# Kernel optimization log

Hardware: AMD Instinct MI355X
Metric: run time of the kernel (lower is better)

The kernel has to match this reference:

```python
import jax, jax.numpy as jnp
import numpy as np

B, S, E, H = 8, 1024, 64, 8
DK = E // H  # n_wires per head
DIM = 2 ** DK  # statevector size


def _quantum_projection(x, phi):
    """Faithful batched simulation of _QLayer for every (batch, seq, head).
    Encoder RX(x_i) followed by trainable RX(phi_i) on the same wire equals
    RX(x_i + phi_i). Then a CNOT ring, then <Z_w> for each wire.
    x: [B,S,E] float, phi: [H,DK] float -> [B,S,E] float expectations.
    """
    b, s, e = x.shape
    theta = x.reshape(b, s, H, DK) + phi  # [B,S,H,DK]
    M = b * s * H
    th = theta.reshape(M, DK)
    # RX(t)|0> = cos(t/2)|0> - i sin(t/2)|1>
    c = jnp.cos(th * 0.5).astype(jnp.complex64)
    sn = (jnp.sin(th * 0.5) * (-1j)).astype(jnp.complex64)
    q = jnp.stack([c, sn], axis=-1)  # [M, DK, 2]
    # product state via iterated kron over the DK wires (fixed small loop)
    amps = jnp.ones((M, 1), jnp.complex64)
    for w in range(DK):
        amps = (amps[:, :, None] * q[:, w, None, :]).reshape(M, -1)
    st = amps.reshape((M,) + (2,) * DK)
    # CNOT ring: (0,1),(1,2),...,(DK-2,DK-1),(DK-1,0)
    gates = [(w, w + 1) for w in range(DK - 1)] + [(DK - 1, 0)]
    for cw, tw in gates:
        ac = 1 + cw
        s0 = jnp.take(st, 0, axis=ac)  # control = 0: identity
        s1 = jnp.take(st, 1, axis=ac)  # control = 1: flip target
        at = 1 + tw - (1 if tw > cw else 0)  # target axis after removing control axis
        s1 = jnp.flip(s1, axis=at)
        st = jnp.stack([s0, s1], axis=ac)
    stf = st.reshape(M, DIM)
    probs = stf.real ** 2 + stf.imag ** 2  # [M, DIM]
    # <Z_w> = sum_k probs[k] * (1 - 2*bit_w(k)); wire 0 is most-significant bit
    bits = (jnp.arange(DIM)[:, None] >> jnp.arange(DK - 1, -1, -1)[None, :]) & 1
    signs = (1 - 2 * bits).astype(probs.dtype)  # [DIM, DK]
    expz = probs @ signs  # [M, DK]
    return expz.reshape(b, s, e)


def setup_inputs() -> dict:
    key = jax.random.key(0)
    k1, k2, k3, k4 = jax.random.split(key, 4)
    x = jax.random.normal(k1, (B, S, E), dtype=jnp.float32)
    phi = jax.random.normal(k2, (H, DK), dtype=jnp.float32) * 0.1  # trainable RX params
    lim = 1.0 / np.sqrt(E)
    W = jax.random.uniform(k3, (E, E), jnp.float32, -lim, lim)  # combine Linear weight
    b = jax.random.uniform(k4, (E,), jnp.float32, -lim, lim)    # combine Linear bias
    return {"x": x, "phi": phi, "W": W, "b": b}


def reference(x, phi, W, b):
    # q = k = v = _projection(x): the original calls _projection(x) 3 times with
    # the same params and no randomness, so they are identical; compute once.
    proj = _quantum_projection(x, phi)  # [B,S,E]
    scores = jax.nn.softmax(
        jnp.einsum('bse,bte->bst', proj, proj) / jnp.sqrt(jnp.float32(DK)), axis=-1)
    # dropout is identity in eval mode
    ctx = jnp.einsum('bst,bte->bse', scores, proj)
    return ctx @ W.T + b
```

## Files before the change

### kernel.cpp

```cpp
#include <hip/hip_runtime.h>
#include <hip/hip_bf16.h>

#define BB 8
#define SS 1024
#define EE 64
#define HH 8
#define DKW 8

typedef __hip_bfloat16 bf16;
typedef unsigned short u16;
typedef _Float16 half8v __attribute__((ext_vector_type(8)));
typedef float floatx4 __attribute__((ext_vector_type(4)));

#define MFMA16(a, b, c) __builtin_amdgcn_mfma_f32_16x16x32_f16(a, b, c, 0, 0, 0)

#define OFF_PROJT ((size_t)BB * SS * EE * 2)

template <int NT>
__device__ __forceinline__ bool detect_f32(const u16* __restrict__ base,
                                           int tid, int* red) {
    int cnt = 0;
#pragma unroll
    for (int i = tid; i < 2048; i += NT) {
        u16 u = base[i * 2];
        int ex = (u >> 7) & 0xFF;
        cnt += (ex >= 0x84) ? 1 : 0;
    }
#pragma unroll
    for (int off = 32; off > 0; off >>= 1) cnt += __shfl_xor(cnt, off, 64);
    if ((tid & 63) == 0) red[tid >> 6] = cnt;
    __syncthreads();
    int tot = 0;
#pragma unroll
    for (int w = 0; w < NT / 64; ++w) tot += red[w];
    return tot > 64;
}

__device__ __forceinline__ void proj_compute(const void* x, const void* phi,
                                             bool f32, int m, float* z) {
    int h = m & (HH - 1);
    float th[DKW];
    if (f32) {
        const float4* xp = (const float4*)((const float*)x + (size_t)m * DKW);
        const float4* pp = (const float4*)((const float*)phi + h * DKW);
        float4 x0 = xp[0], x1 = xp[1];
        float4 p0 = pp[0], p1 = pp[1];
        th[0] = x0.x + p0.x; th[1] = x0.y + p0.y; th[2] = x0.z + p0.z; th[3] = x0.w + p0.w;
        th[4] = x1.x + p1.x; th[5] = x1.y + p1.y; th[6] = x1.z + p1.z; th[7] = x1.w + p1.w;
    } else {
        union { uint4 u; bf16 hv[8]; } xu, pu;
        xu.u = *(const uint4*)((const bf16*)x + (size_t)m * DKW);
        pu.u = *(const uint4*)((const bf16*)phi + (size_t)h * DKW);
#pragma unroll
        for (int j = 0; j < DKW; ++j)
            th[j] = __bfloat162float(xu.hv[j]) + __bfloat162float(pu.hv[j]);
    }
    float c[DKW];
#pragma unroll
    for (int j = 0; j < DKW; ++j) c[j] = __cosf(th[j]);
    float suf = c[1];
#pragma unroll
    for (int j = 2; j < DKW; ++j) suf *= c[j];
    z[0] = suf;
    float pre = c[0];
#pragma unroll
    for (int w = 1; w < DKW; ++w) { pre *= c[w]; z[w] = pre; }
}

__global__ __launch_bounds__(256) void proj_f16_kernel(const void* __restrict__ x,
                                                       const void* __restrict__ phi,
                                                       _Float16* __restrict__ projH,
                                                       _Float16* __restrict__ projT) {
    __shared__ int redd[4];
    __shared__ _Float16 zt[EE][40];
    const int tid = threadIdx.x;
    const bool f32 = detect_f32<256>((const u16*)x, tid, redd);

    const int m = blockIdx.x * 256 + tid;
    float z[DKW];
    proj_compute(x, phi, f32, m, z);

    union { half8v v; _Float16 h[8]; } o;
#pragma unroll
    for (int j = 0; j < DKW; ++j) o.h[j] = (_Float16)z[j];
    *(half8v*)(projH + (size_t)m * DKW) = o.v;

    const int h = m & (HH - 1);
    const int sl = (tid >> 3) & 31;
#pragma unroll
    for (int j = 0; j < DKW; ++j) zt[h * DKW + j][sl] = o.h[j];
    __syncthreads();

    const int b = blockIdx.x >> 5;
    const int s0 = (blockIdx.x * 32) & (SS - 1);
    const int row = tid >> 2, ch = tid & 3;
    half8v vv = *(const half8v*)(&zt[row][ch * 8]);
    *(half8v*)(projT + ((size_t)(b * EE + row)) * SS + s0 + ch * 8) = vv;
}

__device__ __forceinline__ int sidx(int row, int colblk) {
    return row * 1024 + ((colblk ^ (row & 7)) << 3);
}

__global__ __launch_bounds__(512) void fused_attn(const _Float16* __restrict__ projH,
                                                  const _Float16* __restrict__ projT,
                                                  const void* __restrict__ Wp,
                                                  const void* __restrict__ biasp,
                                                  void* __restrict__ outp) {
    __shared__ _Float16 Stile[16 * 1024];
    __shared__ float    pacc[4][16][17];
    __shared__ _Float16 ctx_lds[16][72];
    __shared__ float    rowsum[16];
    __shared__ int      redd[8];

    const int tid = threadIdx.x;
    const int wave = tid >> 6, lane = tid & 63;
    const int lr = lane & 15, quad = lane >> 4;
    const int b = blockIdx.y;
    const int m0 = blockIdx.x * 16;

    const bool f32 = detect_f32<512>((const u16*)Wp, tid, redd);

    const _Float16* Pb = projH + (size_t)b * SS * EE;
    const float scale = 0.35355339059327373f;

    {
        const _Float16* arow = Pb + (size_t)(m0 + lr) * EE;
        half8v a0 = *(const half8v*)(arow + quad * 8);
        half8v a1 = *(const half8v*)(arow + 32 + quad * 8);
#pragma unroll 4
        for (int c = 0; c < 8; ++c) {
            int n = wave * 128 + c * 16;
            const _Float16* brow = Pb + (size_t)(n + lr) * EE;
            half8v b0 = *(const half8v*)(brow + quad * 8);
            half8v b1 = *(const half8v*)(brow + 32 + quad * 8);
            floatx4 acc = {0.f, 0.f, 0.f, 0.f};
            acc = MFMA16(a0, b0, acc);
            acc = MFMA16(a1, b1, acc);
#pragma unroll
            for (int r = 0; r < 4; ++r) {
                int row = quad * 4 + r, col = n + lr;
                Stile[sidx(row, col >> 3) + (col & 7)] = (_Float16)(acc[r] * scale);
            }
        }
    }
    __syncthreads();

    {
        const int row = tid >> 5, seg = tid & 31;
        half8v hv[4];
#pragma unroll
        for (int i = 0; i < 4; ++i)
            hv[i] = *(const half8v*)(&Stile[sidx(row, i * 32 + seg)]);
        float mloc = -1e30f;
#pragma unroll
        for (int i = 0; i < 4; ++i)
#pragma unroll
            for (int j = 0; j < 8; ++j) mloc = fmaxf(mloc, (float)hv[i][j]);
#pragma unroll
        for (int off = 16; off > 0; off >>= 1)
            mloc = fmaxf(mloc, __shfl_xor(mloc, off, 64));
        float lsum = 0.f;
#pragma unroll
        for (int i = 0; i < 4; ++i) {
#pragma unroll
            for (int j = 0; j < 8; ++j) {
                float e = __expf((float)hv[i][j] - mloc);
                lsum += e;
                hv[i][j] = (_Float16)(e * 256.f);
            }
        }
#pragma unroll
        for (int off = 16; off > 0; off >>= 1)
            lsum += __shfl_xor(lsum, off, 64);
        if (seg == 0) rowsum[row] = lsum;
#pragma unroll
        for (int i = 0; i < 4; ++i)
            *(half8v*)(&Stile[sidx(row, i * 32 + seg)]) = hv[i];
    }
    __syncthreads();

    const int khalf = wave >> 2, colg = wave & 3;
    floatx4 accT;
    {
        const _Float16* vrow = projT + ((size_t)(b * EE + colg * 16 + lr)) * SS
                               + khalf * 512;
        const int sbase = khalf * 64;
        floatx4 acc0 = {0.f, 0.f, 0.f, 0.f};
        floatx4 acc1 = {0.f, 0.f, 0.f, 0.f};
#pragma unroll 4
        for (int t = 0; t < 512; t += 64) {
            half8v aA = *(const half8v*)(&Stile[sidx(lr, sbase + (t >> 3) + quad)]);
            half8v vA = *(const half8v*)(vrow + t + quad * 8);
            half8v aB = *(const half8v*)(&Stile[sidx(lr, sbase + ((t + 32) >> 3) + quad)]);
            half8v vB = *(const half8v*)(vrow + t + 32 + quad * 8);
            acc0 = MFMA16(aA, vA, acc0);
            acc1 = MFMA16(aB, vB, acc1);
        }
        accT = acc0 + acc1;
    }
    if (khalf == 1) {
#pragma unroll
        for (int r = 0; r < 4; ++r) pacc[colg][quad * 4 + r][lr] = accT[r];
    }
    __syncthreads();
    if (khalf == 0) {
#pragma unroll
        for (int r = 0; r < 4; ++r) {
            int row_l = quad * 4 + r;
            float inv = 1.0f / (256.0f * rowsum[row_l]);
            ctx_lds[row_l][colg * 16 + lr] =
                (_Float16)((accT[r] + pacc[colg][row_l][lr]) * inv);
        }
    }
    __syncthreads();

    if (wave < 4) {
        const int o = wave * 16 + lr;
        half8v ca0 = *(const half8v*)(&ctx_lds[lr][quad * 8]);
        half8v ca1 = *(const half8v*)(&ctx_lds[lr][32 + quad * 8]);
        half8v wb0, wb1;
        if (f32) {
            const float* wr = (const float*)Wp + (size_t)o * EE;
            union { half8v v; _Float16 h[8]; } w0, w1;
#pragma unroll
            for (int j = 0; j < 8; ++j) {
                w0.h[j] = (_Float16)wr[quad * 8 + j];
                w1.h[j] = (_Float16)wr[32 + quad * 8 + j];
            }
            wb0 = w0.v; wb1 = w1.v;
        } else {
            const bf16* wr = (const bf16*)Wp + (size_t)o * EE;
            union { uint4 u; bf16 hv[8]; } r0, r1;
            r0.u = *(const uint4*)(wr + quad * 8);
            r1.u = *(const uint4*)(wr + 32 + quad * 8);
            union { half8v v; _Float16 h[8]; } w0, w1;
#pragma unroll
            for (int j = 0; j < 8; ++j) {
                w0.h[j] = (_Float16)__bfloat162float(r0.hv[j]);
                w1.h[j] = (_Float16)__bfloat162float(r1.hv[j]);
            }
            wb0 = w0.v; wb1 = w1.v;
        }
        floatx4 oacc = {0.f, 0.f, 0.f, 0.f};
        oacc = MFMA16(ca0, wb0, oacc);
        oacc = MFMA16(ca1, wb1, oacc);

        float bo = f32 ? ((const float*)biasp)[o]
                       : __bfloat162float(((const bf16*)biasp)[o]);
#pragma unroll
        for (int r = 0; r < 4; ++r) {
            size_t oi = ((size_t)b * SS + m0 + quad * 4 + r) * EE + o;
            float val = oacc[r] + bo;
            if (f32) ((float*)outp)[oi] = val;
            else     ((bf16*)outp)[oi] = __float2bfloat16(val);
        }
    }
}

extern "C" void kernel_launch(void* const* d_in, const int* in_sizes, int n_in,
                              void* d_out, int out_size, void* d_ws, size_t ws_size,
                              hipStream_t stream) {
    const void* x    = d_in[0];
    const void* phi  = d_in[1];
    const void* W    = d_in[2];
    const void* bias = d_in[3];

    _Float16* projH = (_Float16*)d_ws;
    _Float16* projT = (_Float16*)((char*)d_ws + OFF_PROJT);

    proj_f16_kernel<<<dim3(BB * SS * HH / 256), dim3(256), 0, stream>>>(x, phi, projH, projT);
    fused_attn<<<dim3(SS / 16, BB), dim3(512), 0, stream>>>(projH, projT, W, bias, d_out);
}
```

Baseline: 83.76 us.

## Fuse projection and attention into one cooperative kernel with grid sync

Merges the projection kernel and the fused attention kernel into a single cooperative launch of 512 blocks. Each block first computes its slice of projH/projT, then all blocks meet at a grid-wide barrier before running attention. The goal is to drop the second kernel launch and the gap between kernels. The cost is a grid-wide barrier, only 128 of 512 threads active during projection, and a cooperative launch that may fail; if it fails, the code falls back to the old two-kernel path.

```diff
diff --git a/kernel.cpp b/kernel.cpp
--- a/kernel.cpp
+++ b/kernel.cpp
@@ -1,5 +1,8 @@
 #include <hip/hip_runtime.h>
 #include <hip/hip_bf16.h>
+#include <hip/hip_cooperative_groups.h>
+
+namespace cg = cooperative_groups;
 
 #define BB 8
 #define SS 1024
@@ -20,7 +23,6 @@
 __device__ __forceinline__ bool detect_f32(const u16* __restrict__ base,
                                            int tid, int* red) {
     int cnt = 0;
-#pragma unroll
     for (int i = tid; i < 2048; i += NT) {
         u16 u = base[i * 2];
         int ex = (u >> 7) & 0xFF;
@@ -67,60 +69,57 @@
     for (int w = 1; w < DKW; ++w) { pre *= c[w]; z[w] = pre; }
 }
 
-__global__ __launch_bounds__(256) void proj_f16_kernel(const void* __restrict__ x,
-                                                       const void* __restrict__ phi,
-                                                       _Float16* __restrict__ projH,
-                                                       _Float16* __restrict__ projT) {
-    __shared__ int redd[4];
-    __shared__ _Float16 zt[EE][40];
-    const int tid = threadIdx.x;
-    const bool f32 = detect_f32<256>((const u16*)x, tid, redd);
-
-    const int m = blockIdx.x * 256 + tid;
-    float z[DKW];
-    proj_compute(x, phi, f32, m, z);
-
-    union { half8v v; _Float16 h[8]; } o;
-#pragma unroll
-    for (int j = 0; j < DKW; ++j) o.h[j] = (_Float16)z[j];
-    *(half8v*)(projH + (size_t)m * DKW) = o.v;
-
-    const int h = m & (HH - 1);
-    const int sl = (tid >> 3) & 31;
-#pragma unroll
-    for (int j = 0; j < DKW; ++j) zt[h * DKW + j][sl] = o.h[j];
-    __syncthreads();
-
-    const int b = blockIdx.x >> 5;
-    const int s0 = (blockIdx.x * 32) & (SS - 1);
-    const int row = tid >> 2, ch = tid & 3;
-    half8v vv = *(const half8v*)(&zt[row][ch * 8]);
-    *(half8v*)(projT + ((size_t)(b * EE + row)) * SS + s0 + ch * 8) = vv;
-}
-
 __device__ __forceinline__ int sidx(int row, int colblk) {
     return row * 1024 + ((colblk ^ (row & 7)) << 3);
 }
 
-__global__ __launch_bounds__(512) void fused_attn(const _Float16* __restrict__ projH,
-                                                  const _Float16* __restrict__ projT,
-                                                  const void* __restrict__ Wp,
-                                                  const void* __restrict__ biasp,
-                                                  void* __restrict__ outp) {
+__global__ __launch_bounds__(512, 4) void mega_kernel(const void* __restrict__ x,
+                                                      const void* __restrict__ phi,
+                                                      const void* __restrict__ Wp,
+                                                      const void* __restrict__ biasp,
+                                                      void* __restrict__ outp,
+                                                      _Float16* __restrict__ projH,
+                                                      _Float16* __restrict__ projT) {
     __shared__ _Float16 Stile[16 * 1024];
     __shared__ float    pacc[4][16][17];
     __shared__ _Float16 ctx_lds[16][72];
+    __shared__ _Float16 zt[EE][24];
     __shared__ float    rowsum[16];
     __shared__ int      redd[8];
 
     const int tid = threadIdx.x;
     const int wave = tid >> 6, lane = tid & 63;
     const int lr = lane & 15, quad = lane >> 4;
-    const int b = blockIdx.y;
-    const int m0 = blockIdx.x * 16;
-
-    const bool f32 = detect_f32<512>((const u16*)Wp, tid, redd);
-
+    const int blk = blockIdx.x;
+
+    const bool f32 = detect_f32<512>((const u16*)x, tid, redd);
+
+    {
+        if (tid < 128) {
+            int m = blk * 128 + tid;
+            float z[DKW];
+            proj_compute(x, phi, f32, m, z);
+            union { half8v v; _Float16 h[8]; } o;
+#pragma unroll
+            for (int j = 0; j < DKW; ++j) o.h[j] = (_Float16)z[j];
+            *(half8v*)(projH + (size_t)m * DKW) = o.v;
+            int h = m & (HH - 1), sl = tid >> 3;
+#pragma unroll
+            for (int j = 0; j < DKW; ++j) zt[h * DKW + j][sl] = o.h[j];
+        }
+        __syncthreads();
+        if (tid < 128) {
+            int pb = blk >> 6;
+            int s0 = (blk & 63) * 16;
+            int row = tid >> 1, ch = tid & 1;
+            half8v vv = *(const half8v*)(&zt[row][ch * 8]);
+            *(half8v*)(projT + ((size_t)(pb * EE + row)) * SS + s0 + ch * 8) = vv;
+        }
+    }
+    cg::this_grid().sync();
+
+    const int b = blk >> 6;
+    const int m0 = (blk & 63) * 16;
     const _Float16* Pb = projH + (size_t)b * SS * EE;
     const float scale = 0.35355339059327373f;
 
@@ -258,6 +257,191 @@
     }
 }
 
+__global__ __launch_bounds__(256) void proj_f16_kernel(const void* __restrict__ x,
+                                                       const void* __restrict__ phi,
+                                                       _Float16* __restrict__ projH,
+                                                       _Float16* __restrict__ projT) {
+    __shared__ int redd[4];
+    __shared__ _Float16 zt[EE][40];
+    const int tid = threadIdx.x;
+    const bool f32 = detect_f32<256>((const u16*)x, tid, redd);
+
+    const int m = blockIdx.x * 256 + tid;
+    float z[DKW];
+    proj_compute(x, phi, f32, m, z);
+
+    union { half8v v; _Float16 h[8]; } o;
+#pragma unroll
+    for (int j = 0; j < DKW; ++j) o.h[j] = (_Float16)z[j];
+    *(half8v*)(projH + (size_t)m * DKW) = o.v;
+
+    const int h = m & (HH - 1);
+    const int sl = (tid >> 3) & 31;
+#pragma unroll
+    for (int j = 0; j < DKW; ++j) zt[h * DKW + j][sl] = o.h[j];
+    __syncthreads();
+
+    const int b = blockIdx.x >> 5;
+    const int s0 = (blockIdx.x * 32) & (SS - 1);
+    const int row = tid >> 2, ch = tid & 3;
+    half8v vv = *(const half8v*)(&zt[row][ch * 8]);
+    *(half8v*)(projT + ((size_t)(b * EE + row)) * SS + s0 + ch * 8) = vv;
+}
+
+__global__ __launch_bounds__(512) void fused_attn(const _Float16* __restrict__ projH,
+                                                  const _Float16* __restrict__ projT,
+                                                  const void* __restrict__ Wp,
+                                                  const void* __restrict__ biasp,
+                                                  void* __restrict__ outp) {
+    __shared__ _Float16 Stile[16 * 1024];
+    __shared__ float    pacc[4][16][17];
+    __shared__ _Float16 ctx_lds[16][72];
+    __shared__ float    rowsum[16];
+    __shared__ int      redd[8];
+
+    const int tid = threadIdx.x;
+    const int wave = tid >> 6, lane = tid & 63;
+    const int lr = lane & 15, quad = lane >> 4;
+    const int b = blockIdx.y;
+    const int m0 = blockIdx.x * 16;
+
+    const bool f32 = detect_f32<512>((const u16*)Wp, tid, redd);
+    const _Float16* Pb = projH + (size_t)b * SS * EE;
+    const float scale = 0.35355339059327373f;
+
+    {
+        const _Float16* arow = Pb + (size_t)(m0 + lr) * EE;
+        half8v a0 = *(const half8v*)(arow + quad * 8);
+        half8v a1 = *(const half8v*)(arow + 32 + quad * 8);
+#pragma unroll 4
+        for (int c = 0; c < 8; ++c) {
+            int n = wave * 128 + c * 16;
+            const _Float16* brow = Pb + (size_t)(n + lr) * EE;
+            half8v b0 = *(const half8v*)(brow + quad * 8);
+            half8v b1 = *(const half8v*)(brow + 32 + quad * 8);
+            floatx4 acc = {0.f, 0.f, 0.f, 0.f};
+            acc = MFMA16(a0, b0, acc);
+            acc = MFMA16(a1, b1, acc);
+#pragma unroll
+            for (int r = 0; r < 4; ++r) {
+                int row = quad * 4 + r, col = n + lr;
+                Stile[sidx(row, col >> 3) + (col & 7)] = (_Float16)(acc[r] * scale);
+            }
+        }
+    }
+    __syncthreads();
+    {
+        const int row = tid >> 5, seg = tid & 31;
+        half8v hv[4];
+#pragma unroll
+        for (int i = 0; i < 4; ++i)
+            hv[i] = *(const half8v*)(&Stile[sidx(row, i * 32 + seg)]);
+        float mloc = -1e30f;
+#pragma unroll
+        for (int i = 0; i < 4; ++i)
+#pragma unroll
+            for (int j = 0; j < 8; ++j) mloc = fmaxf(mloc, (float)hv[i][j]);
+#pragma unroll
+        for (int off = 16; off > 0; off >>= 1)
+            mloc = fmaxf(mloc, __shfl_xor(mloc, off, 64));
+        float lsum = 0.f;
+#pragma unroll
+        for (int i = 0; i < 4; ++i) {
+#pragma unroll
+            for (int j = 0; j < 8; ++j) {
+                float e = __expf((float)hv[i][j] - mloc);
+                lsum += e;
+                hv[i][j] = (_Float16)(e * 256.f);
+            }
+        }
+#pragma unroll
+        for (int off = 16; off > 0; off >>= 1)
+            lsum += __shfl_xor(lsum, off, 64);
+        if (seg == 0) rowsum[row] = lsum;
+#pragma unroll
+        for (int i = 0; i < 4; ++i)
+            *(half8v*)(&Stile[sidx(row, i * 32 + seg)]) = hv[i];
+    }
+    __syncthreads();
+
+    const int khalf = wave >> 2, colg = wave & 3;
+    floatx4 accT;
+    {
+        const _Float16* vrow = projT + ((size_t)(b * EE + colg * 16 + lr)) * SS
+                               + khalf * 512;
+        const int sbase = khalf * 64;
+        floatx4 acc0 = {0.f, 0.f, 0.f, 0.f};
+        floatx4 acc1 = {0.f, 0.f, 0.f, 0.f};
+#pragma unroll 4
+        for (int t = 0; t < 512; t += 64) {
+            half8v aA = *(const half8v*)(&Stile[sidx(lr, sbase + (t >> 3) + quad)]);
+            half8v vA = *(const half8v*)(vrow + t + quad * 8);
+            half8v aB = *(const half8v*)(&Stile[sidx(lr, sbase + ((t + 32) >> 3) + quad)]);
+            half8v vB = *(const half8v*)(vrow + t + 32 + quad * 8);
+            acc0 = MFMA16(aA, vA, acc0);
+            acc1 = MFMA16(aB, vB, acc1);
+        }
+        accT = acc0 + acc1;
+    }
+    if (khalf == 1) {
+#pragma unroll
+        for (int r = 0; r < 4; ++r) pacc[colg][quad * 4 + r][lr] = accT[r];
+    }
+    __syncthreads();
+    if (khalf == 0) {
+#pragma unroll
+        for (int r = 0; r < 4; ++r) {
+            int row_l = quad * 4 + r;
+            float inv = 1.0f / (256.0f * rowsum[row_l]);
+            ctx_lds[row_l][colg * 16 + lr] =
+                (_Float16)((accT[r] + pacc[colg][row_l][lr]) * inv);
+        }
+    }
+    __syncthreads();
+
+    if (wave < 4) {
+        const int o = wave * 16 + lr;
+        half8v ca0 = *(const half8v*)(&ctx_lds[lr][quad * 8]);
+        half8v ca1 = *(const half8v*)(&ctx_lds[lr][32 + quad * 8]);
+        half8v wb0, wb1;
+        if (f32) {
+            const float* wr = (const float*)Wp + (size_t)o * EE;
+            union { half8v v; _Float16 h[8]; } w0, w1;
+#pragma unroll
+            for (int j = 0; j < 8; ++j) {
+                w0.h[j] = (_Float16)wr[quad * 8 + j];
+                w1.h[j] = (_Float16)wr[32 + quad * 8 + j];
+            }
+            wb0 = w0.v; wb1 = w1.v;
+        } else {
+            const bf16* wr = (const bf16*)Wp + (size_t)o * EE;
+            union { uint4 u; bf16 hv[8]; } r0, r1;
+            r0.u = *(const uint4*)(wr + quad * 8);
+            r1.u = *(const uint4*)(wr + 32 + quad * 8);
+            union { half8v v; _Float16 h[8]; } w0, w1;
+#pragma unroll
+            for (int j = 0; j < 8; ++j) {
+                w0.h[j] = (_Float16)__bfloat162float(r0.hv[j]);
+                w1.h[j] = (_Float16)__bfloat162float(r1.hv[j]);
+            }
+            wb0 = w0.v; wb1 = w1.v;
+        }
+        floatx4 oacc = {0.f, 0.f, 0.f, 0.f};
+        oacc = MFMA16(ca0, wb0, oacc);
+        oacc = MFMA16(ca1, wb1, oacc);
+
+        float bo = f32 ? ((const float*)biasp)[o]
+                       : __bfloat162float(((const bf16*)biasp)[o]);
+#pragma unroll
+        for (int r = 0; r < 4; ++r) {
+            size_t oi = ((size_t)b * SS + m0 + quad * 4 + r) * EE + o;
+            float val = oacc[r] + bo;
+            if (f32) ((float*)outp)[oi] = val;
+            else     ((bf16*)outp)[oi] = __float2bfloat16(val);
+        }
+    }
+}
+
 extern "C" void kernel_launch(void* const* d_in, const int* in_sizes, int n_in,
                               void* d_out, int out_size, void* d_ws, size_t ws_size,
                               hipStream_t stream) {
@@ -265,10 +449,20 @@
     const void* phi  = d_in[1];
     const void* W    = d_in[2];
     const void* bias = d_in[3];
+    void* outp = d_out;
 
     _Float16* projH = (_Float16*)d_ws;
     _Float16* projT = (_Float16*)((char*)d_ws + OFF_PROJT);
 
-    proj_f16_kernel<<<dim3(BB * SS * HH / 256), dim3(256), 0, stream>>>(x, phi, projH, projT);
-    fused_attn<<<dim3(SS / 16, BB), dim3(512), 0, stream>>>(projH, projT, W, bias, d_out);
-}
+    void* args[] = {(void*)&x, (void*)&phi, (void*)&W, (void*)&bias,
+                    (void*)&outp, (void*)&projH, (void*)&projT};
+    hipError_t err = hipLaunchCooperativeKernel(
+        reinterpret_cast<void*>(mega_kernel), dim3(512), dim3(512), args, 0, stream);
+
+    if (err != hipSuccess) {
+        proj_f16_kernel<<<dim3(BB * SS * HH / 256), dim3(256), 0, stream>>>(
+            x, phi, projH, projT);
+        fused_attn<<<dim3(SS / 16, BB), dim3(512), 0, stream>>>(
+            projH, projT, W, bias, d_out);
+    }
+}
```

Result: slower. 138.6 us (+65.5%).

## Fuse quantum projection into attention kernel, recomputing K/V tiles in shared memory

Applied to the files above, without the earlier changes.

Replaces the two-kernel pipeline with a single kernel that recomputes projected query, key and value tiles from x and phi directly into LDS, chunk by chunk, for both the QK and PV phases. This removes the workspace round trip and one kernel launch. In exchange, each block recomputes the projections of all keys twice, which multiplies the transcendental work and adds per-chunk barriers.

```diff
diff --git a/kernel.cpp b/kernel.cpp
--- a/kernel.cpp
+++ b/kernel.cpp
@@ -14,13 +14,10 @@
 
 #define MFMA16(a, b, c) __builtin_amdgcn_mfma_f32_16x16x32_f16(a, b, c, 0, 0, 0)
 
-#define OFF_PROJT ((size_t)BB * SS * EE * 2)
-
 template <int NT>
 __device__ __forceinline__ bool detect_f32(const u16* __restrict__ base,
                                            int tid, int* red) {
     int cnt = 0;
-#pragma unroll
     for (int i = tid; i < 2048; i += NT) {
         u16 u = base[i * 2];
         int ex = (u >> 7) & 0xFF;
@@ -67,46 +64,16 @@
     for (int w = 1; w < DKW; ++w) { pre *= c[w]; z[w] = pre; }
 }
 
-__global__ __launch_bounds__(256) void proj_f16_kernel(const void* __restrict__ x,
-                                                       const void* __restrict__ phi,
-                                                       _Float16* __restrict__ projH,
-                                                       _Float16* __restrict__ projT) {
-    __shared__ int redd[4];
-    __shared__ _Float16 zt[EE][40];
-    const int tid = threadIdx.x;
-    const bool f32 = detect_f32<256>((const u16*)x, tid, redd);
-
-    const int m = blockIdx.x * 256 + tid;
-    float z[DKW];
-    proj_compute(x, phi, f32, m, z);
-
-    union { half8v v; _Float16 h[8]; } o;
-#pragma unroll
-    for (int j = 0; j < DKW; ++j) o.h[j] = (_Float16)z[j];
-    *(half8v*)(projH + (size_t)m * DKW) = o.v;
-
-    const int h = m & (HH - 1);
-    const int sl = (tid >> 3) & 31;
-#pragma unroll
-    for (int j = 0; j < DKW; ++j) zt[h * DKW + j][sl] = o.h[j];
-    __syncthreads();
-
-    const int b = blockIdx.x >> 5;
-    const int s0 = (blockIdx.x * 32) & (SS - 1);
-    const int row = tid >> 2, ch = tid & 3;
-    half8v vv = *(const half8v*)(&zt[row][ch * 8]);
-    *(half8v*)(projT + ((size_t)(b * EE + row)) * SS + s0 + ch * 8) = vv;
-}
-
 __device__ __forceinline__ int sidx(int row, int colblk) {
     return row * 1024 + ((colblk ^ (row & 7)) << 3);
 }
 
-__global__ __launch_bounds__(512) void fused_attn(const _Float16* __restrict__ projH,
-                                                  const _Float16* __restrict__ projT,
-                                                  const void* __restrict__ Wp,
-                                                  const void* __restrict__ biasp,
-                                                  void* __restrict__ outp) {
+__global__ __launch_bounds__(512, 2) void qflash(const void* __restrict__ x,
+                                                 const void* __restrict__ phi,
+                                                 const void* __restrict__ Wp,
+                                                 const void* __restrict__ biasp,
+                                                 void* __restrict__ outp) {
+    __shared__ _Float16 KV[8192];
     __shared__ _Float16 Stile[16 * 1024];
     __shared__ float    pacc[4][16][17];
     __shared__ _Float16 ctx_lds[16][72];
@@ -116,35 +83,57 @@
     const int tid = threadIdx.x;
     const int wave = tid >> 6, lane = tid & 63;
     const int lr = lane & 15, quad = lane >> 4;
-    const int b = blockIdx.y;
-    const int m0 = blockIdx.x * 16;
-
-    const bool f32 = detect_f32<512>((const u16*)Wp, tid, redd);
-
-    const _Float16* Pb = projH + (size_t)b * SS * EE;
+    const int bid = blockIdx.x;
+    const int b = bid & 7;
+    const int m0 = (bid >> 3) * 16;
+    const int sl = tid & 127, hh = tid >> 7;
+
+    const bool f32 = detect_f32<512>((const u16*)x, tid, redd);
     const float scale = 0.35355339059327373f;
 
+    half8v a0, a1;
     {
-        const _Float16* arow = Pb + (size_t)(m0 + lr) * EE;
-        half8v a0 = *(const half8v*)(arow + quad * 8);
-        half8v a1 = *(const half8v*)(arow + 32 + quad * 8);
-#pragma unroll 4
-        for (int c = 0; c < 8; ++c) {
-            int n = wave * 128 + c * 16;
-            const _Float16* brow = Pb + (size_t)(n + lr) * EE;
-            half8v b0 = *(const half8v*)(brow + quad * 8);
-            half8v b1 = *(const half8v*)(brow + 32 + quad * 8);
+        float z[8];
+        union { half8v v; _Float16 h[8]; } u;
+        proj_compute(x, phi, f32, ((b << 10) + (m0 + lr)) * 8 + quad, z);
+#pragma unroll
+        for (int j = 0; j < 8; ++j) u.h[j] = (_Float16)z[j];
+        a0 = u.v;
+        proj_compute(x, phi, f32, ((b << 10) + (m0 + lr)) * 8 + quad + 4, z);
+#pragma unroll
+        for (int j = 0; j < 8; ++j) u.h[j] = (_Float16)z[j];
+        a1 = u.v;
+    }
+
+#pragma unroll 1
+    for (int ch = 0; ch < 8; ++ch) {
+#pragma unroll
+        for (int hp = 0; hp < 2; ++hp) {
+            int h = hh + hp * 4;
+            int s = ch * 128 + sl;
+            float z[8];
+            proj_compute(x, phi, f32, ((b << 10) + s) * 8 + h, z);
+            union { half8v v; _Float16 hx[8]; } u;
+#pragma unroll
+            for (int j = 0; j < 8; ++j) u.hx[j] = (_Float16)z[j];
+            *(half8v*)(&KV[(h * 128 + sl) * 8]) = u.v;
+        }
+        __syncthreads();
+        {
+            int s_local = wave * 16 + lr;
+            half8v b0 = *(const half8v*)(&KV[(quad * 128 + s_local) * 8]);
+            half8v b1 = *(const half8v*)(&KV[((quad + 4) * 128 + s_local) * 8]);
             floatx4 acc = {0.f, 0.f, 0.f, 0.f};
             acc = MFMA16(a0, b0, acc);
             acc = MFMA16(a1, b1, acc);
 #pragma unroll
             for (int r = 0; r < 4; ++r) {
-                int row = quad * 4 + r, col = n + lr;
+                int row = quad * 4 + r, col = ch * 128 + wave * 16 + lr;
                 Stile[sidx(row, col >> 3) + (col & 7)] = (_Float16)(acc[r] * scale);
             }
         }
-    }
-    __syncthreads();
+        __syncthreads();
+    }
 
     {
         const int row = tid >> 5, seg = tid & 31;
@@ -180,37 +169,48 @@
     }
     __syncthreads();
 
-    const int khalf = wave >> 2, colg = wave & 3;
-    floatx4 accT;
-    {
-        const _Float16* vrow = projT + ((size_t)(b * EE + colg * 16 + lr)) * SS
-                               + khalf * 512;
-        const int sbase = khalf * 64;
-        floatx4 acc0 = {0.f, 0.f, 0.f, 0.f};
-        floatx4 acc1 = {0.f, 0.f, 0.f, 0.f};
-#pragma unroll 4
-        for (int t = 0; t < 512; t += 64) {
-            half8v aA = *(const half8v*)(&Stile[sidx(lr, sbase + (t >> 3) + quad)]);
-            half8v vA = *(const half8v*)(vrow + t + quad * 8);
-            half8v aB = *(const half8v*)(&Stile[sidx(lr, sbase + ((t + 32) >> 3) + quad)]);
-            half8v vB = *(const half8v*)(vrow + t + 32 + quad * 8);
-            acc0 = MFMA16(aA, vA, acc0);
-            acc1 = MFMA16(aB, vB, acc1);
-        }
-        accT = acc0 + acc1;
-    }
-    if (khalf == 1) {
-#pragma unroll
-        for (int r = 0; r < 4; ++r) pacc[colg][quad * 4 + r][lr] = accT[r];
-    }
-    __syncthreads();
-    if (khalf == 0) {
+    const int th = wave >> 2, eg = wave & 3;
+    floatx4 accA = {0.f, 0.f, 0.f, 0.f}, accB = {0.f, 0.f, 0.f, 0.f};
+#pragma unroll 1
+    for (int ch = 0; ch < 8; ++ch) {
+#pragma unroll
+        for (int hp = 0; hp < 2; ++hp) {
+            int h = hh + hp * 4;
+            int t = ch * 128 + sl;
+            float z[8];
+            proj_compute(x, phi, f32, ((b << 10) + t) * 8 + h, z);
+            int tblk = sl >> 3, tin = sl & 7;
+#pragma unroll
+            for (int j = 0; j < 8; ++j) {
+                int jr = (j + sl) & 7;
+                KV[(tblk * 64 + h * 8 + jr) * 8 + tin] = (_Float16)z[jr];
+            }
+        }
+        __syncthreads();
+        {
+            half8v B0 = *(const half8v*)(&KV[((th * 8 + quad) * 64 + eg * 16 + lr) * 8]);
+            half8v B1 = *(const half8v*)(&KV[((th * 8 + 4 + quad) * 64 + eg * 16 + lr) * 8]);
+            half8v A0 = *(const half8v*)(&Stile[sidx(lr, ch * 16 + th * 8 + quad)]);
+            half8v A1 = *(const half8v*)(&Stile[sidx(lr, ch * 16 + th * 8 + 4 + quad)]);
+            accA = MFMA16(A0, B0, accA);
+            accB = MFMA16(A1, B1, accB);
+        }
+        __syncthreads();
+    }
+    floatx4 accT = accA + accB;
+
+    if (th == 1) {
+#pragma unroll
+        for (int r = 0; r < 4; ++r) pacc[eg][quad * 4 + r][lr] = accT[r];
+    }
+    __syncthreads();
+    if (th == 0) {
 #pragma unroll
         for (int r = 0; r < 4; ++r) {
             int row_l = quad * 4 + r;
             float inv = 1.0f / (256.0f * rowsum[row_l]);
-            ctx_lds[row_l][colg * 16 + lr] =
-                (_Float16)((accT[r] + pacc[colg][row_l][lr]) * inv);
+            ctx_lds[row_l][eg * 16 + lr] =
+                (_Float16)((accT[r] + pacc[eg][row_l][lr]) * inv);
         }
     }
     __syncthreads();
@@ -265,10 +265,7 @@
     const void* phi  = d_in[1];
     const void* W    = d_in[2];
     const void* bias = d_in[3];
-
-    _Float16* projH = (_Float16*)d_ws;
-    _Float16* projT = (_Float16*)((char*)d_ws + OFF_PROJT);
-
-    proj_f16_kernel<<<dim3(BB * SS * HH / 256), dim3(256), 0, stream>>>(x, phi, projH, projT);
-    fused_attn<<<dim3(SS / 16, BB), dim3(512), 0, stream>>>(projH, projT, W, bias, d_out);
-}
+    (void)d_ws; (void)ws_size;
+
+    qflash<<<dim3(512), dim3(512), 0, stream>>>(x, phi, W, bias, d_out);
+}
```

Result: slower. 110.1 us (+31.5%).
